# Kernel optimization log

Measured on AMD Instinct MI355X. Metric: run time of the kernel, lower is better.

The kernel has to match this reference:

```python
import jax, jax.numpy as jnp
import numpy as np

NUM_HEADS = 16
HEAD_DIM = 64
MAX_POS = 1024


def setup_inputs() -> dict:
    key = jax.random.key(0)
    ks = jax.random.split(key, 8)
    B, S, Hd = 4, 1024, 1024
    return {
        "hidden_states": jax.random.normal(ks[0], (B, S, Hd), dtype=jnp.float32),
        "wq": jax.random.normal(ks[1], (Hd, Hd), dtype=jnp.float32) * 0.02,
        "bq": jax.random.normal(ks[2], (Hd,), dtype=jnp.float32) * 0.02,
        "wk": jax.random.normal(ks[3], (Hd, Hd), dtype=jnp.float32) * 0.02,
        "bk": jax.random.normal(ks[4], (Hd,), dtype=jnp.float32) * 0.02,
        "wv": jax.random.normal(ks[5], (Hd, Hd), dtype=jnp.float32) * 0.02,
        "bv": jax.random.normal(ks[6], (Hd,), dtype=jnp.float32) * 0.02,
        "dist_emb": jax.random.normal(ks[7], (2 * MAX_POS - 1, HEAD_DIM), dtype=jnp.float32) * 0.02,
    }


def _heads(x):
    # [B, S, H*d] -> [B, H, S, d]
    B, S, _ = x.shape
    return x.reshape(B, S, NUM_HEADS, HEAD_DIM).transpose(0, 2, 1, 3)


def reference(hidden_states, wq, bq, wk, bk, wv, bv, dist_emb):
    B, S, Hd = hidden_states.shape
    q = _heads(hidden_states @ wq.T + bq)  # [B,H,S,d]
    k = _heads(hidden_states @ wk.T + bk)
    v = _heads(hidden_states @ wv.T + bv)

    scores = jnp.einsum("bhsd,bhtd->bhst", q, k)  # [B,H,S,S]

    # relative_key_query positional bias
    pos = jnp.arange(S)
    distance = pos[:, None] - pos[None, :] + (MAX_POS - 1)  # [S,S]
    pe = dist_emb[distance]  # [S,S,d]
    scores = scores + jnp.einsum("bhld,lrd->bhlr", q, pe) + jnp.einsum("bhrd,lrd->bhlr", k, pe)

    scores = scores / jnp.sqrt(jnp.float32(HEAD_DIM)).astype(scores.dtype)
    probs = jax.nn.softmax(scores, axis=-1)

    ctx = jnp.einsum("bhst,bhtd->bhsd", probs, v)  # [B,H,S,d]
    return ctx.transpose(0, 2, 1, 3).reshape(B, S, Hd)
```

## Files before the change

kernel.cpp:

```cpp
#include <hip/hip_runtime.h>

typedef __attribute__((ext_vector_type(8))) short bf16x8;
typedef __attribute__((ext_vector_type(4))) float f32x4;

#define L2E 1.44269504088896340736f

__device__ __forceinline__ unsigned short f2bf(float x) {
    union { float f; unsigned u; } v; v.f = x;
    return (unsigned short)((v.u + 0x7FFFu + ((v.u >> 16) & 1u)) >> 16);
}
__device__ __forceinline__ float bf2f(unsigned short b) {
    union { unsigned u; float f; } v; v.u = ((unsigned)b) << 16;
    return v.f;
}

#define GLDS(gp, lp) __builtin_amdgcn_global_load_lds( \
    (const __attribute__((address_space(1))) unsigned int*)(const void*)(gp), \
    (__attribute__((address_space(3))) unsigned int*)(void*)(lp), 16, 0, 0)

__global__ void cvt_bf16(const float* __restrict__ src, unsigned short* __restrict__ dst, int n4) {
    int i = blockIdx.x * blockDim.x + threadIdx.x;
    if (i < n4) {
        float4 v = reinterpret_cast<const float4*>(src)[i];
        ushort4 o;
        o.x = f2bf(v.x); o.y = f2bf(v.y); o.z = f2bf(v.z); o.w = f2bf(v.w);
        reinterpret_cast<ushort4*>(dst)[i] = o;
    }
}

__global__ __launch_bounds__(256, 2) void qkv_proj(
    const unsigned short* __restrict__ A,
    const unsigned short* __restrict__ W,
    const float* __restrict__ bq, const float* __restrict__ bk, const float* __restrict__ bv,
    unsigned short* __restrict__ q_ws, unsigned short* __restrict__ k_ws, unsigned short* __restrict__ v_ws)
{
    __shared__ __align__(16) unsigned short Al[128 * 64];
    __shared__ __align__(16) unsigned short Bl[128 * 64];
    const int mt = blockIdx.x, nt = blockIdx.y;
    const int tid = threadIdx.x, w = tid >> 6, l = tid & 63;
    const int m0 = mt * 128, n0 = nt * 128;
    const int lg = l >> 4, ll = l & 15;
    const int lrow8 = l >> 3, lchunk = l & 7;

    f32x4 acc[4][4] = {};

    for (int kt = 0; kt < 16; ++kt) {
        __syncthreads();
        #pragma unroll
        for (int t = 0; t < 4; ++t) {
            int roff = (w * 4 + t) * 8 + lrow8;
            int sch = lchunk ^ (roff & 7);
            GLDS(A + (m0 + roff) * 1024 + kt * 64 + sch * 8, Al + (w * 4 + t) * 512);
            GLDS(W + (n0 + roff) * 1024 + kt * 64 + sch * 8, Bl + (w * 4 + t) * 512);
        }
        __syncthreads();
        #pragma unroll
        for (int kk = 0; kk < 2; ++kk) {
            const int cb = kk * 4 + lg;
            bf16x8 af[4], bfr[4];
            #pragma unroll
            for (int fr = 0; fr < 4; ++fr) {
                int row = (w >> 1) * 64 + fr * 16 + ll;
                af[fr] = *reinterpret_cast<const bf16x8*>(Al + row * 64 + ((cb ^ (row & 7)) << 3));
            }
            #pragma unroll
            for (int fc = 0; fc < 4; ++fc) {
                int row = (w & 1) * 64 + fc * 16 + ll;
                bfr[fc] = *reinterpret_cast<const bf16x8*>(Bl + row * 64 + ((cb ^ (row & 7)) << 3));
            }
            #pragma unroll
            for (int fr = 0; fr < 4; ++fr)
                #pragma unroll
                for (int fc = 0; fc < 4; ++fc)
                    acc[fr][fc] = __builtin_amdgcn_mfma_f32_16x16x32_bf16(af[fr], bfr[fc], acc[fr][fc], 0, 0, 0);
        }
    }

    const int matrix = n0 >> 10;
    const float* bias = matrix == 0 ? bq : (matrix == 1 ? bk : bv);
    unsigned short* dst = matrix == 0 ? q_ws : (matrix == 1 ? k_ws : v_ws);
    #pragma unroll
    for (int fc = 0; fc < 4; ++fc) {
        int nloc = (w & 1) * 64 + fc * 16 + ll;
        int o = (n0 + nloc) & 1023;
        float bb = bias[o];
        int h = o >> 6, dd = o & 63;
        #pragma unroll
        for (int fr = 0; fr < 4; ++fr) {
            int rbase = (w >> 1) * 64 + fr * 16 + (lg << 2);
            #pragma unroll
            for (int e = 0; e < 4; ++e) {
                int mg = m0 + rbase + e;
                int b = mg >> 10, s = mg & 1023;
                int bh = b * 16 + h;
                unsigned short val = f2bf(acc[fr][fc][e] + bb);
                if (matrix < 2) dst[(bh * 1024 + s) * 64 + dd] = val;
                else            dst[(bh * 64 + dd) * 1024 + s] = val;
            }
        }
    }
}

__global__ __launch_bounds__(256, 2) void git_attn(
    const unsigned short* __restrict__ q_ws,
    const unsigned short* __restrict__ k_ws,
    const unsigned short* __restrict__ v_ws,
    const unsigned short* __restrict__ Dbf,
    float* __restrict__ out)
{
    __shared__ __align__(16) char smem[75776];
    unsigned short* K_l  = (unsigned short*)(smem);
    unsigned short* Vt_l = (unsigned short*)(smem + 8192);
    unsigned short* Dw_l = (unsigned short*)(smem + 16384);
    unsigned short* QDt  = (unsigned short*)(smem + 32768);
    unsigned short* KDt  = (unsigned short*)(smem + 50176);
    unsigned short* P_l  = (unsigned short*)(smem + 67584);

    const int qt = blockIdx.x, bh = blockIdx.y;
    const int l0 = qt * 64;
    const int tid = threadIdx.x, w = tid >> 6, l = tid & 63;
    const int lg = l >> 4, ll = l & 15;
    const int lrow8 = l >> 3, lchunk = l & 7;

    const unsigned short* qb = q_ws + bh * 65536;
    const unsigned short* kb = k_ws + bh * 65536;
    const unsigned short* vb = v_ws + bh * 65536;

    bf16x8 qf[2];
    {
        int row = l0 + 16 * w + ll;
        qf[0] = *reinterpret_cast<const bf16x8*>(qb + row * 64 + lg * 8);
        qf[1] = *reinterpret_cast<const bf16x8*>(qb + row * 64 + lg * 8 + 32);
    }

    f32x4 Oacc[4] = {};
    float mrow[4] = {-1e30f, -1e30f, -1e30f, -1e30f};
    float lrow[4] = {};
    unsigned short* Pw = P_l + w * 1024;

    for (int rt = 0; rt < 16; ++rt) {
        const int r0 = rt * 64;
        const int m0 = l0 - r0 + 960;
        __syncthreads();
        #pragma unroll
        for (int t = 0; t < 2; ++t) {
            int row = (w * 2 + t) * 8 + lrow8;
            int sch = lchunk ^ (row & 7);
            GLDS(kb + (r0 + row) * 64 + sch * 8, K_l + (w * 2 + t) * 512);
            GLDS(vb + row * 1024 + r0 + sch * 8, Vt_l + (w * 2 + t) * 512);
        }
        #pragma unroll
        for (int t = 0; t < 4; ++t) {
            int row = (w * 4 + t) * 8 + lrow8;
            int srow = m0 + row; srow = srow > 2046 ? 2046 : srow;
            int sch = lchunk ^ (row & 7);
            GLDS(Dbf + srow * 64 + sch * 8, Dw_l + (w * 4 + t) * 512);
        }
        __syncthreads();

        f32x4 Sacc[4] = {};
        bf16x8 kaf[2];
        #pragma unroll
        for (int kk = 0; kk < 2; ++kk) {
            const int cb = kk * 4 + lg;
            #pragma unroll
            for (int jt = 0; jt < 4; ++jt) {
                int row = jt * 16 + ll;
                bf16x8 kf = *reinterpret_cast<const bf16x8*>(K_l + row * 64 + ((cb ^ (row & 7)) << 3));
                Sacc[jt] = __builtin_amdgcn_mfma_f32_16x16x32_bf16(qf[kk], kf, Sacc[jt], 0, 0, 0);
            }
            int row = 16 * w + ll;
            kaf[kk] = *reinterpret_cast<const bf16x8*>(K_l + row * 64 + ((cb ^ (row & 7)) << 3));
        }
        f32x4 QDacc[8] = {}; f32x4 KDacc[8] = {};
        #pragma unroll
        for (int kk = 0; kk < 2; ++kk) {
            const int cb = kk * 4 + lg;
            #pragma unroll
            for (int tt = 0; tt < 8; ++tt) {
                int row = tt * 16 + ll;
                bf16x8 df = *reinterpret_cast<const bf16x8*>(Dw_l + row * 64 + ((cb ^ (row & 7)) << 3));
                QDacc[tt] = __builtin_amdgcn_mfma_f32_16x16x32_bf16(qf[kk],  df, QDacc[tt], 0, 0, 0);
                KDacc[tt] = __builtin_amdgcn_mfma_f32_16x16x32_bf16(kaf[kk], df, KDacc[tt], 0, 0, 0);
            }
        }
        {
            int i0 = 16 * w + (lg << 2);
            #pragma unroll
            for (int tt = 0; tt < 8; ++tt) {
                int t = ll + 16 * tt;
                ushort4 qa, ka;
                qa.x = f2bf(QDacc[tt][0]); qa.y = f2bf(QDacc[tt][1]); qa.z = f2bf(QDacc[tt][2]); qa.w = f2bf(QDacc[tt][3]);
                ka.x = f2bf(KDacc[tt][0]); ka.y = f2bf(KDacc[tt][1]); ka.z = f2bf(KDacc[tt][2]); ka.w = f2bf(KDacc[tt][3]);
                *reinterpret_cast<ushort4*>(QDt + t * 68 + i0) = qa;
                *reinterpret_cast<ushort4*>(KDt + t * 68 + i0) = ka;
            }
        }
        __syncthreads();

        float pvv[4][4];
        float rm[4] = {-1e30f, -1e30f, -1e30f, -1e30f};
        #pragma unroll
        for (int jt = 0; jt < 4; ++jt) {
            int j = ll + 16 * jt;
            #pragma unroll
            for (int e = 0; e < 4; ++e) {
                int i = 16 * w + (lg << 2) + e;
                int t = i - j + 63;
                float sv = (Sacc[jt][e] + bf2f(QDt[t * 68 + i]) + bf2f(KDt[t * 68 + j])) * 0.125f;
                pvv[jt][e] = sv;
                rm[e] = fmaxf(rm[e], sv);
            }
        }
        #pragma unroll
        for (int e = 0; e < 4; ++e) {
            #pragma unroll
            for (int msk = 1; msk < 16; msk <<= 1)
                rm[e] = fmaxf(rm[e], __shfl_xor(rm[e], msk, 64));
        }
        float psum[4];
        #pragma unroll
        for (int e = 0; e < 4; ++e) {
            float mn = fmaxf(mrow[e], rm[e]);
            float sc = exp2f((mrow[e] - mn) * L2E);
            mrow[e] = mn;
            lrow[e] *= sc;
            #pragma unroll
            for (int dt = 0; dt < 4; ++dt) Oacc[dt][e] *= sc;
            float ps = 0.f;
            #pragma unroll
            for (int jt = 0; jt < 4; ++jt) {
                float p = exp2f((pvv[jt][e] - mn) * L2E);
                pvv[jt][e] = p;
                ps += p;
            }
            psum[e] = ps;
        }
        #pragma unroll
        for (int e = 0; e < 4; ++e) {
            #pragma unroll
            for (int msk = 1; msk < 16; msk <<= 1)
                psum[e] += __shfl_xor(psum[e], msk, 64);
            lrow[e] += psum[e];
        }
        #pragma unroll
        for (int jt = 0; jt < 4; ++jt) {
            int j = ll + 16 * jt;
            #pragma unroll
            for (int e = 0; e < 4; ++e) {
                int i16 = (lg << 2) + e;
                Pw[i16 * 64 + (((j >> 3) ^ (i16 & 7)) << 3) + (j & 7)] = f2bf(pvv[jt][e]);
            }
        }
        #pragma unroll
        for (int jj = 0; jj < 2; ++jj) {
            const int cb = jj * 4 + lg;
            bf16x8 pf = *reinterpret_cast<const bf16x8*>(Pw + ll * 64 + ((cb ^ (ll & 7)) << 3));
            #pragma unroll
            for (int dt = 0; dt < 4; ++dt) {
                int row = dt * 16 + ll;
                bf16x8 vf = *reinterpret_cast<const bf16x8*>(Vt_l + row * 64 + ((cb ^ (row & 7)) << 3));
                Oacc[dt] = __builtin_amdgcn_mfma_f32_16x16x32_bf16(pf, vf, Oacc[dt], 0, 0, 0);
            }
        }
    }

    const int b = bh >> 4, h = bh & 15;
    #pragma unroll
    for (int e = 0; e < 4; ++e) {
        float inv = 1.f / lrow[e];
        int s = l0 + 16 * w + (lg << 2) + e;
        #pragma unroll
        for (int dt = 0; dt < 4; ++dt) {
            int d = ll + 16 * dt;
            out[((b * 1024 + s) * 16 + h) * 64 + d] = Oacc[dt][e] * inv;
        }
    }
}

extern "C" void kernel_launch(void* const* d_in, const int* in_sizes, int n_in,
                              void* d_out, int out_size, void* d_ws, size_t ws_size,
                              hipStream_t stream) {
    const float* hs = (const float*)d_in[0];
    const float* wq = (const float*)d_in[1];
    const float* bq = (const float*)d_in[2];
    const float* wk = (const float*)d_in[3];
    const float* bk = (const float*)d_in[4];
    const float* wv = (const float*)d_in[5];
    const float* bv = (const float*)d_in[6];
    const float* de = (const float*)d_in[7];
    float* out = (float*)d_out;
    char* ws = (char*)d_ws;

    unsigned short* hs_bf = (unsigned short*)(ws);
    unsigned short* w_bf  = (unsigned short*)(ws + 8388608);
    unsigned short* D_bf  = (unsigned short*)(ws + 14680064);
    unsigned short* q_ws  = (unsigned short*)(ws + 14942208);
    unsigned short* k_ws  = (unsigned short*)(ws + 23330816);
    unsigned short* v_ws  = (unsigned short*)(ws + 31719424);

    int n4;
    n4 = 4096 * 1024 / 4;
    cvt_bf16<<<(n4 + 255) / 256, 256, 0, stream>>>(hs, hs_bf, n4);
    n4 = 1024 * 1024 / 4;
    cvt_bf16<<<(n4 + 255) / 256, 256, 0, stream>>>(wq, w_bf,           n4);
    cvt_bf16<<<(n4 + 255) / 256, 256, 0, stream>>>(wk, w_bf + 1048576, n4);
    cvt_bf16<<<(n4 + 255) / 256, 256, 0, stream>>>(wv, w_bf + 2097152, n4);
    n4 = 2047 * 64 / 4;
    cvt_bf16<<<(n4 + 255) / 256, 256, 0, stream>>>(de, D_bf, n4);

    qkv_proj<<<dim3(32, 24), 256, 0, stream>>>(hs_bf, w_bf, bq, bk, bv, q_ws, k_ws, v_ws);
    git_attn<<<dim3(16, 64), 256, 0, stream>>>(q_ws, k_ws, v_ws, D_bf, out);
}
```

Baseline: 255.7 us.

## Stage QKV projection epilogue through swizzled LDS for vectorized stores

The QKV projection epilogue now writes bf16 results into shared memory with an XOR swizzle, then reads them back as 16-byte rows and issues coalesced uint4 global stores, including a transposed layout for V. This replaces scattered 2-byte global stores. The change also remaps block indices so tiles that share weights run closer together, and raises the launch-bounds occupancy hint from 2 to 3. The cost is an extra LDS round-trip and two barriers, plus possible register pressure from the higher occupancy target.

```diff
diff --git a/kernel.cpp b/kernel.cpp
--- a/kernel.cpp
+++ b/kernel.cpp
@@ -28,15 +28,20 @@
     }
 }
 
-__global__ __launch_bounds__(256, 2) void qkv_proj(
+__global__ __launch_bounds__(256, 3) void qkv_proj(
     const unsigned short* __restrict__ A,
     const unsigned short* __restrict__ W,
     const float* __restrict__ bq, const float* __restrict__ bk, const float* __restrict__ bv,
     unsigned short* __restrict__ q_ws, unsigned short* __restrict__ k_ws, unsigned short* __restrict__ v_ws)
 {
-    __shared__ __align__(16) unsigned short Al[128 * 64];
-    __shared__ __align__(16) unsigned short Bl[128 * 64];
-    const int mt = blockIdx.x, nt = blockIdx.y;
+    __shared__ __align__(16) unsigned short Lds[16384];
+    unsigned short* Al = Lds;
+    unsigned short* Bl = Lds + 8192;
+
+    const int lin = blockIdx.x + 32 * blockIdx.y;
+    const int lp = (lin & 7) * 96 + (lin >> 3);
+    const int mt = lp & 31, nt = lp >> 5;
+
     const int tid = threadIdx.x, w = tid >> 6, l = tid & 63;
     const int m0 = mt * 128, n0 = nt * 128;
     const int lg = l >> 4, ll = l & 15;
@@ -79,24 +84,56 @@
     const int matrix = n0 >> 10;
     const float* bias = matrix == 0 ? bq : (matrix == 1 ? bk : bv);
     unsigned short* dst = matrix == 0 ? q_ws : (matrix == 1 ? k_ws : v_ws);
+
+    __syncthreads();
+
+    if (matrix < 2) {
+        #pragma unroll
+        for (int fc = 0; fc < 4; ++fc) {
+            int nloc = (w & 1) * 64 + fc * 16 + ll;
+            float bb = bias[(n0 + nloc) & 1023];
+            #pragma unroll
+            for (int fr = 0; fr < 4; ++fr) {
+                #pragma unroll
+                for (int e = 0; e < 4; ++e) {
+                    int m = (w >> 1) * 64 + fr * 16 + (lg << 2) + e;
+                    Lds[m * 128 + (((nloc >> 3) ^ (m & 15)) << 3) + (nloc & 7)] =
+                        f2bf(acc[fr][fc][e] + bb);
+                }
+            }
+        }
+    } else {
+        #pragma unroll
+        for (int fc = 0; fc < 4; ++fc) {
+            int nloc = (w & 1) * 64 + fc * 16 + ll;
+            float bb = bias[(n0 + nloc) & 1023];
+            #pragma unroll
+            for (int fr = 0; fr < 4; ++fr) {
+                int mb = (w >> 1) * 64 + fr * 16 + (lg << 2);
+                ushort4 pk;
+                pk.x = f2bf(acc[fr][fc][0] + bb);
+                pk.y = f2bf(acc[fr][fc][1] + bb);
+                pk.z = f2bf(acc[fr][fc][2] + bb);
+                pk.w = f2bf(acc[fr][fc][3] + bb);
+                *reinterpret_cast<ushort4*>(Lds + nloc * 128 + (((mb >> 3) ^ (nloc & 15)) << 3) + (mb & 7)) = pk;
+            }
+        }
+    }
+    __syncthreads();
+
     #pragma unroll
-    for (int fc = 0; fc < 4; ++fc) {
-        int nloc = (w & 1) * 64 + fc * 16 + ll;
-        int o = (n0 + nloc) & 1023;
-        float bb = bias[o];
-        int h = o >> 6, dd = o & 63;
-        #pragma unroll
-        for (int fr = 0; fr < 4; ++fr) {
-            int rbase = (w >> 1) * 64 + fr * 16 + (lg << 2);
-            #pragma unroll
-            for (int e = 0; e < 4; ++e) {
-                int mg = m0 + rbase + e;
-                int b = mg >> 10, s = mg & 1023;
-                int bh = b * 16 + h;
-                unsigned short val = f2bf(acc[fr][fc][e] + bb);
-                if (matrix < 2) dst[(bh * 1024 + s) * 64 + dd] = val;
-                else            dst[(bh * 64 + dd) * 1024 + s] = val;
-            }
+    for (int p = 0; p < 8; ++p) {
+        int r = (tid >> 4) + 16 * p;
+        int cc = tid & 15;
+        uint4 val = *reinterpret_cast<const uint4*>(Lds + r * 128 + ((cc ^ (r & 15)) << 3));
+        if (matrix < 2) {
+            int mg = m0 + r;          int b = mg >> 10, s = mg & 1023;
+            int ng = n0 + cc * 8;     int h = (ng & 1023) >> 6, dd = ng & 63;
+            *reinterpret_cast<uint4*>(dst + ((b * 16 + h) * 1024 + s) * 64 + dd) = val;
+        } else {
+            int ng = n0 + r;          int h = (ng & 1023) >> 6, dd = ng & 63;
+            int mg = m0 + cc * 8;     int b = mg >> 10, s = mg & 1023;
+            *reinterpret_cast<uint4*>(dst + (b * 16 + h) * 65536 + dd * 1024 + s) = val;
         }
     }
 }
```

Result: no change. 257.5 us (+0.7%).
